# Kernel optimization log

Hardware: AMD Instinct MI355X
Metric: run time of the kernel (lower is better)

## Reference

```python
import jax, jax.numpy as jnp
import numpy as np

B, N, QD = 2, 2048, 1024
HEADS, DIM_HEAD = 16, 64
INNER = HEADS * DIM_HEAD  # 1024
SCALE = DIM_HEAD ** -0.5


def setup_inputs() -> dict:
    key = jax.random.key(0)
    ks = jax.random.split(key, 8)
    x = jax.random.normal(ks[0], (B, N, QD), dtype=jnp.float32)
    bias = jax.random.normal(ks[1], (B, N, N), dtype=jnp.float32)
    mask = jax.random.randint(ks[2], (B, N), 0, 2) > 0
    # parameters (nn.Linear stores weight [out, in]; we keep [in, out] and matmul x @ W)
    Wq = jax.random.normal(ks[3], (QD, INNER), dtype=jnp.float32) * (QD ** -0.5)
    Wkv = jax.random.normal(ks[4], (QD, 2 * INNER), dtype=jnp.float32) * (QD ** -0.5)
    Wo = jax.random.normal(ks[5], (INNER, QD), dtype=jnp.float32) * (INNER ** -0.5)
    bo = jax.random.normal(ks[6], (QD,), dtype=jnp.float32) * 0.01
    return {"x": x, "bias": bias, "mask": mask, "Wq": Wq, "Wkv": Wkv, "Wo": Wo, "bo": bo}


def reference(x, bias, mask, Wq, Wkv, Wo, bo):
    b, n, _ = x.shape
    q = x @ Wq                      # [b, n, inner]
    kv = x @ Wkv                    # [b, n, 2*inner] (context defaults to x)
    k, v = jnp.split(kv, 2, axis=-1)
    # split heads: [b, h, n, d]
    split = lambda t: t.reshape(b, n, HEADS, DIM_HEAD).transpose(0, 2, 1, 3)
    q, k, v = split(q), split(k), split(v)
    sim = jnp.einsum('bhid,bhjd->bhij', q, k) * SCALE   # [b, h, n, n]
    sim = sim + bias[:, None, :, :]                      # additive bias broadcast over heads
    max_neg = -jnp.finfo(sim.dtype).max
    sim = jnp.where(mask[:, None, None, :], sim, max_neg)  # per-key mask
    attn = jax.nn.softmax(sim, axis=-1)
    out = jnp.einsum('bhij,bhjd->bhid', attn, v)         # [b, h, n, d]
    out = out.transpose(0, 2, 1, 3).reshape(b, n, INNER)  # merge heads
    return out @ Wo + bo
```

## Files before the change

kernel.cpp:

```cpp
#include <hip/hip_runtime.h>
#include <hip/hip_bf16.h>
#include <stdint.h>

#define B_     2
#define N_     2048
#define QD_    1024
#define H_     16
#define DH_    64
#define INNER_ 1024
#define SCALE_ 0.125f

typedef unsigned short u16;
typedef __attribute__((ext_vector_type(8))) short bf16x8;
typedef __attribute__((ext_vector_type(4))) float f32x4;
typedef __attribute__((ext_vector_type(4))) unsigned short u16x4;
typedef __attribute__((ext_vector_type(8))) unsigned short u16x8;

#define GLD16(gp, lp) __builtin_amdgcn_global_load_lds( \
    (const __attribute__((address_space(1))) unsigned int*)(gp), \
    (__attribute__((address_space(3))) unsigned int*)(lp), 16, 0, 0)

__device__ inline u16 f2bf(float f) {
    union { float f; uint32_t u; } c; c.f = f;
    uint32_t r = c.u + 0x7FFFu + ((c.u >> 16) & 1u);
    return (u16)(r >> 16);
}
__device__ inline float bf2f(u16 s) {
    union { uint32_t u; float f; } c; c.u = ((uint32_t)s) << 16;
    return c.f;
}
__device__ inline void split2(float v, u16 &h, u16 &l) {
    u16 hs = f2bf(v);
    h = hs;
    l = f2bf(v - bf2f(hs));
}
__device__ inline unsigned pk2(float a, float b) {
    float2 f; f.x = a; f.y = b;
    union { __hip_bfloat162 v; unsigned u; } c;
    c.v = __float22bfloat162_rn(f);
    return c.u;
}
__device__ inline float f4get(const float4& v, int r) {
    return r == 0 ? v.x : r == 1 ? v.y : r == 2 ? v.z : v.w;
}

__global__ __launch_bounds__(256) void prep_kernel(
    const float* __restrict__ x, u16* __restrict__ xh, u16* __restrict__ xl,
    const float* __restrict__ Wq, const float* __restrict__ Wkv, const float* __restrict__ Wo,
    u16* __restrict__ wTh, u16* __restrict__ wTl,
    u16* __restrict__ woTh, u16* __restrict__ woTl)
{
    __shared__ float t[32][33];
    const int blk = blockIdx.x, tid = threadIdx.x;
    if (blk < 4096) {
        int idx = blk * 256 + tid;
        float4 v = ((const float4*)x)[idx];
        u16x4 hv, lv; u16 h, l;
        split2(v.x, h, l); hv.x = h; lv.x = l;
        split2(v.y, h, l); hv.y = h; lv.y = l;
        split2(v.z, h, l); hv.z = h; lv.z = l;
        split2(v.w, h, l); hv.w = h; lv.w = l;
        ((u16x4*)xh)[idx] = hv;
        ((u16x4*)xl)[idx] = lv;
        return;
    }
    int local = blk - 4096;
    const float* src; u16 *dhi, *dlo; int C, bx, by;
    if (local < 1024)      { src = Wq;  dhi = wTh;                dlo = wTl;                C = 1024; by = local >> 5; bx = local & 31; }
    else if (local < 3072) { int l2 = local - 1024; src = Wkv; dhi = wTh + 1024 * 1024; dlo = wTl + 1024 * 1024; C = 2048; by = l2 >> 6; bx = l2 & 63; }
    else                   { int l2 = local - 3072; src = Wo;  dhi = woTh;               dlo = woTl;               C = 1024; by = l2 >> 5; bx = l2 & 31; }
    const int x0 = bx * 32, y0 = by * 32;
    const int tx = tid & 31, ty = tid >> 5;
    for (int yy = ty; yy < 32; yy += 8)
        t[yy][tx] = src[(size_t)(y0 + yy) * C + x0 + tx];
    __syncthreads();
    for (int i = ty; i < 32; i += 8) {
        float v = t[tx][i];
        u16 h, l; split2(v, h, l);
        size_t o = (size_t)(x0 + i) * 1024 + y0 + tx;
        dhi[o] = h; dlo[o] = l;
    }
}

__device__ inline void bias_read(int T, int bkoff, int bl16,
                                 const float* __restrict__ bias,
                                 const int* __restrict__ mask,
                                 float4 bR[4], int4& bM)
{
    int bb2 = T >> 10, rest = T & 1023;
    int k0b = (rest & 31) * 64, q0 = (rest >> 5) * 64;
    int kk = k0b + bkoff;
    bM = *(const int4*)&mask[bb2 * N_ + kk];
#pragma unroll
    for (int m = 0; m < 4; m++)
        bR[m] = *(const float4*)&bias[((size_t)bb2 * N_ + q0 + m * 16 + bl16) * N_ + kk];
}
__device__ inline void bias_store(int T, int bwvr, int blane, int bhf,
                                  const float4 bR[4], const int4& bM,
                                  u16* __restrict__ bsw)
{
    int bb2 = T >> 10, rest = T & 1023;
    int k0b = (rest & 31) * 64, q0 = (rest >> 5) * 64;
    int wv = ((k0b >> 5) & 3) + bwvr;
    const u16 NEG = f2bf(-1e30f);
    const int mok[4] = { bM.x, bM.y, bM.z, bM.w };
    u16x8 o0, o1;
#pragma unroll
    for (int i = 0; i < 8; i++) {
        int m = i >> 2, r = i & 3;
        o0[i] = mok[r] ? f2bf(f4get(bR[m], r)) : NEG;
    }
#pragma unroll
    for (int i = 0; i < 8; i++) {
        int m = 2 + (i >> 2), r = i & 3;
        o1[i] = mok[r] ? f2bf(f4get(bR[m], r)) : NEG;
    }
    size_t ob = ((((size_t)bb2 * 32 + (q0 >> 6)) * 16 + (k0b >> 7)) * 4 + wv) * 2048
                + (size_t)blane * 32 + bhf * 16;
    *(u16x8*)&bsw[ob]     = o0;
    *(u16x8*)&bsw[ob + 8] = o1;
}

__global__ __launch_bounds__(256) void gemm_qkv_bias(
    int mode,
    const u16* __restrict__ Ah, const u16* __restrict__ Al,
    const u16* __restrict__ Bh,
    u16* __restrict__ qh,
    u16* __restrict__ kb, u16* __restrict__ vT,
    const float* __restrict__ bias, const int* __restrict__ mask,
    u16* __restrict__ bsw)
{
    __shared__ __align__(16) char smem[49152];
    const int tid = threadIdx.x;

    if (mode == 2) {
        const int bid = blockIdx.x;
        const int bp = tid >> 1, bhf = tid & 1;
        const int blane = bp & 63, bquad = blane >> 4, bl16 = blane & 15;
        const int bwvr = bp >> 6;
        const int bkoff = bwvr * 32 + bquad * 8 + bhf * 4;
        float4 bR[4]; int4 bM;
        bias_read(bid, bkoff, bl16, bias, mask, bR, bM);
        bias_store(bid, bwvr, blane, bhf, bR, bM, bsw);
        return;
    }
    const int gid = blockIdx.x;

    const int wave = tid >> 6, lane = tid & 63;
    const int quad = lane >> 4, l16 = lane & 15;
    const int wm = wave >> 1, wn = wave & 1;
    const int bx = gid % 24, by = gid / 24;
    const int bm = by * 128, bn = bx * 128;
    const bool comp = (bx < 8);

    f32x4 acc[4][4];
#pragma unroll
    for (int i = 0; i < 4; i++)
#pragma unroll
        for (int j = 0; j < 4; j++) acc[i][j] = (f32x4){0.f, 0.f, 0.f, 0.f};

    const int row0 = tid >> 2, g4 = tid & 3;
    const int r1 = row0, r2 = row0 + 64;
    const int gc1 = (g4 ^ (r1 & 3)) * 8, gc2 = (g4 ^ (r2 & 3)) * 8;
    const size_t a1 = (size_t)(bm + r1) * 1024 + gc1, a2 = (size_t)(bm + r2) * 1024 + gc2;
    const size_t b1 = (size_t)(bn + r1) * 1024 + gc1, b2 = (size_t)(bn + r2) * 1024 + gc2;
    const int ldsw = wave * 1024;

    auto issue = [&](char* base, int kn) {
        GLD16(Ah + a1 + kn, base + ldsw);
        GLD16(Ah + a2 + kn, base + 4096 + ldsw);
        GLD16(Bh + b1 + kn, base + 16384 + ldsw);
        GLD16(Bh + b2 + kn, base + 20480 + ldsw);
        if (comp) {
            GLD16(Al + a1 + kn, base + 8192 + ldsw);
            GLD16(Al + a2 + kn, base + 12288 + ldsw);
        }
    };

    const int bp = tid >> 1, bhf = tid & 1;
    const int blane = bp & 63, bquad = blane >> 4, bl16 = blane & 15;
    const int bwvr = bp >> 6;
    const int bkoff = bwvr * 32 + bquad * 8 + bhf * 4;
    float4 bR[4]; int4 bM;

    issue(smem, 0);
    int cur = 0;
    for (int k0 = 0; k0 < 1024; k0 += 32) {
        __syncthreads();
        char* cb_ = smem + cur * 24576;
        if (k0 + 32 < 1024) issue(smem + (cur ^ 1) * 24576, k0 + 32);
        if (mode == 1) {
            const int kstep = k0 >> 5;
            if (kstep == 3)  bias_read (gid,        bkoff, bl16, bias, mask, bR, bM);
            if (kstep == 7)  bias_store(gid,        bwvr, blane, bhf, bR, bM, bsw);
            if (kstep == 11) bias_read (gid + 768,  bkoff, bl16, bias, mask, bR, bM);
            if (kstep == 15) bias_store(gid + 768,  bwvr, blane, bhf, bR, bM, bsw);
            if (kstep == 19 && gid < 512) bias_read (gid + 1536, bkoff, bl16, bias, mask, bR, bM);
            if (kstep == 23 && gid < 512) bias_store(gid + 1536, bwvr, blane, bhf, bR, bM, bsw);
        }
        const u16* cAh = (const u16*)cb_;
        const u16* cAl = (const u16*)(cb_ + 8192);
        const u16* cBh = (const u16*)(cb_ + 16384);
        bf16x8 fah[4], fal[4], fbh[4];
#pragma unroll
        for (int s = 0; s < 4; s++) {
            int ra = wm * 64 + s * 16 + l16;
            int rb = wn * 64 + s * 16 + l16;
            int ca = (quad ^ (ra & 3)) * 8;
            int cb = (quad ^ (rb & 3)) * 8;
            fah[s] = *(const bf16x8*)&cAh[ra * 32 + ca];
            fbh[s] = *(const bf16x8*)&cBh[rb * 32 + cb];
            if (comp) fal[s] = *(const bf16x8*)&cAl[ra * 32 + ca];
        }
#pragma unroll
        for (int sm = 0; sm < 4; sm++)
#pragma unroll
            for (int sn = 0; sn < 4; sn++) {
                acc[sm][sn] = __builtin_amdgcn_mfma_f32_16x16x32_bf16(fah[sm], fbh[sn], acc[sm][sn], 0, 0, 0);
                if (comp)
                    acc[sm][sn] = __builtin_amdgcn_mfma_f32_16x16x32_bf16(fal[sm], fbh[sn], acc[sm][sn], 0, 0, 0);
            }
        cur ^= 1;
    }
#pragma unroll
    for (int sm = 0; sm < 4; sm++) {
        int rowb = bm + wm * 64 + sm * 16 + quad * 4;
        int bb = rowb >> 11, i0 = rowb & 2047;
#pragma unroll
        for (int sn = 0; sn < 4; sn++) {
            int col = bn + wn * 64 + sn * 16 + l16;
            int region = col >> 10;
            int hh = (col >> 6) & 15;
            int d = col & 63;
            if (region == 0) {
#pragma unroll
                for (int r = 0; r < 4; r++) {
                    size_t o = (((size_t)(bb * H_ + hh)) * N_ + i0 + r) * DH_ + d;
                    qh[o] = f2bf(acc[sm][sn][r] * SCALE_);
                }
            } else if (region == 1) {
#pragma unroll
                for (int r = 0; r < 4; r++) {
                    size_t o = (((size_t)(bb * H_ + hh)) * N_ + i0 + r) * DH_ + d;
                    kb[o] = f2bf(acc[sm][sn][r]);
                }
            } else {
                u16x4 pv;
#pragma unroll
                for (int r = 0; r < 4; r++) pv[r] = f2bf(acc[sm][sn][r]);
                *(u16x4*)&vT[(((size_t)(bb * H_ + hh)) * DH_ + d) * N_ + i0] = pv;
            }
        }
    }
}

__global__ __launch_bounds__(256) void gemm_out(
    const u16* __restrict__ Ab,
    const u16* __restrict__ Bh,
    const float* __restrict__ bo, float* __restrict__ out)
{
    __shared__ __align__(16) char smem[24576];
    const int tid = threadIdx.x;
    const int wave = tid >> 6, lane = tid & 63;
    const int quad = lane >> 4, l16 = lane & 15;
    const int wm = wave >> 1, wn = wave & 1;
    const int bm = blockIdx.y * 128, bn = blockIdx.x * 64;

    f32x4 acc[4][2];
#pragma unroll
    for (int i = 0; i < 4; i++)
#pragma unroll
        for (int j = 0; j < 2; j++) acc[i][j] = (f32x4){0.f, 0.f, 0.f, 0.f};

    const int row0 = tid >> 2, g4 = tid & 3;
    const int r1 = row0, r2 = row0 + 64;
    const int gc1 = (g4 ^ (r1 & 3)) * 8, gc2 = (g4 ^ (r2 & 3)) * 8;
    const size_t a1 = (size_t)(bm + r1) * 1024 + gc1, a2 = (size_t)(bm + r2) * 1024 + gc2;
    const size_t bgo = (size_t)(bn + r1) * 1024 + gc1;
    const int ldsw = wave * 1024;

    auto issue = [&](char* base, int kn) {
        GLD16(Ab + a1 + kn, base + ldsw);
        GLD16(Ab + a2 + kn, base + 4096 + ldsw);
        GLD16(Bh + bgo + kn, base + 8192 + ldsw);
    };

    issue(smem, 0);
    int cur = 0;
    for (int k0 = 0; k0 < 1024; k0 += 32) {
        __syncthreads();
        char* cb_ = smem + cur * 12288;
        if (k0 + 32 < 1024) issue(smem + (cur ^ 1) * 12288, k0 + 32);
        const u16* cA  = (const u16*)cb_;
        const u16* cBh = (const u16*)(cb_ + 8192);
        bf16x8 fa[4], fbh[2];
#pragma unroll
        for (int s = 0; s < 4; s++) {
            int ra = wm * 64 + s * 16 + l16;
            int ca = (quad ^ (ra & 3)) * 8;
            fa[s] = *(const bf16x8*)&cA[ra * 32 + ca];
        }
#pragma unroll
        for (int s = 0; s < 2; s++) {
            int rb = wn * 32 + s * 16 + l16;
            int cb = (quad ^ (rb & 3)) * 8;
            fbh[s] = *(const bf16x8*)&cBh[rb * 32 + cb];
        }
#pragma unroll
        for (int sm = 0; sm < 4; sm++)
#pragma unroll
            for (int sn = 0; sn < 2; sn++)
                acc[sm][sn] = __builtin_amdgcn_mfma_f32_16x16x32_bf16(fa[sm], fbh[sn], acc[sm][sn], 0, 0, 0);
        cur ^= 1;
    }
#pragma unroll
    for (int sm = 0; sm < 4; sm++) {
        int rowb = bm + wm * 64 + sm * 16 + quad * 4;
#pragma unroll
        for (int sn = 0; sn < 2; sn++) {
            int col = bn + wn * 32 + sn * 16 + l16;
            float bv = bo[col];
#pragma unroll
            for (int r = 0; r < 4; r++)
                out[(size_t)(rowb + r) * 1024 + col] = acc[sm][sn][r] + bv;
        }
    }
}

__global__ __launch_bounds__(256, 2) void attn_kernel(
    const u16* __restrict__ qh,
    const u16* __restrict__ kb, const u16* __restrict__ vT,
    const u16* __restrict__ bsw, u16* __restrict__ ob)
{
    __shared__ __align__(16) char smem[35328];
    float* rO = (float*)smem;
    float* rL = (float*)(smem + 34816);

    const int bh = blockIdx.y, b = bh >> 4, h = bh & 15;
    const int qt = blockIdx.x, qbase = qt * 64;
    const int tid = threadIdx.x, wave = tid >> 6, lane = tid & 63;
    const int quad = lane >> 4, l16 = lane & 15;

    bf16x8 aq[4][2];
#pragma unroll
    for (int m = 0; m < 4; m++) {
        size_t qo = ((size_t)bh * N_ + qbase + m * 16 + l16) * DH_ + quad * 8;
        aq[m][0] = *(const bf16x8*)&qh[qo];
        aq[m][1] = *(const bf16x8*)&qh[qo + 32];
    }
    f32x4 Oacc[4][4], lacc[4];
#pragma unroll
    for (int m = 0; m < 4; m++) {
        lacc[m] = (f32x4){0.f, 0.f, 0.f, 0.f};
#pragma unroll
        for (int nd = 0; nd < 4; nd++) Oacc[m][nd] = (f32x4){0.f, 0.f, 0.f, 0.f};
    }
    bf16x8 ones;
#pragma unroll
    for (int i = 0; i < 8; i++) ones[i] = (short)0x3F80;

    const int kperm = (l16 >> 2) * 8 + (l16 & 3);
    const size_t kbase0 = ((size_t)bh * N_ + wave * 32 + kperm) * DH_ + quad * 8;
    const size_t vbase0 = ((size_t)bh * DH_ + l16) * N_ + (wave * 4 + quad) * 8;
    const size_t bswb = (size_t)(b * 32 + qt) * 131072 + (size_t)wave * 2048
                        + (size_t)lane * 32;

    bf16x8 kc[2][2], vc[4];
    u16x8 cB[4];
#pragma unroll
    for (int n = 0; n < 2; n++)
#pragma unroll
        for (int s = 0; s < 2; s++)
            kc[n][s] = *(const bf16x8*)&kb[kbase0 + (size_t)(n * 4) * DH_ + s * 32];
#pragma unroll
    for (int nd = 0; nd < 4; nd++)
        vc[nd] = *(const bf16x8*)&vT[vbase0 + (size_t)(nd * 16) * N_];
#pragma unroll
    for (int c = 0; c < 4; c++) cB[c] = *(const u16x8*)&bsw[bswb + c * 8];

#pragma unroll
    for (int jt = 0; jt < 16; jt++) {
        bf16x8 kn_[2][2], vn_[4]; u16x8 nB[4];
        if (jt < 15) {
            int j0n = (jt + 1) * 128;
#pragma unroll
            for (int n = 0; n < 2; n++)
#pragma unroll
                for (int s = 0; s < 2; s++)
                    kn_[n][s] = *(const bf16x8*)&kb[kbase0 + (size_t)(j0n + n * 4) * DH_ + s * 32];
#pragma unroll
            for (int nd = 0; nd < 4; nd++)
                vn_[nd] = *(const bf16x8*)&vT[vbase0 + (size_t)(nd * 16) * N_ + j0n];
            size_t bb = bswb + (size_t)(jt + 1) * 8192;
#pragma unroll
            for (int c = 0; c < 4; c++) nB[c] = *(const u16x8*)&bsw[bb + c * 8];
        }
#pragma unroll
        for (int m = 0; m < 4; m++) {
            f32x4 S0 = (f32x4){0.f, 0.f, 0.f, 0.f};
            f32x4 S1 = (f32x4){0.f, 0.f, 0.f, 0.f};
#pragma unroll
            for (int s = 0; s < 2; s++) {
                S0 = __builtin_amdgcn_mfma_f32_16x16x32_bf16(kc[0][s], aq[m][s], S0, 0, 0, 0);
                S1 = __builtin_amdgcn_mfma_f32_16x16x32_bf16(kc[1][s], aq[m][s], S1, 0, 0, 0);
            }
            float p0[4], p1[4];
#pragma unroll
            for (int r = 0; r < 4; r++) {
                p0[r] = __expf(S0[r] + bf2f(cB[m >> 1][(m & 1) * 4 + r]));
                p1[r] = __expf(S1[r] + bf2f(cB[2 + (m >> 1)][(m & 1) * 4 + r]));
            }
            union { bf16x8 v; unsigned w[4]; } pa;
            pa.w[0] = pk2(p0[0], p0[1]);
            pa.w[1] = pk2(p0[2], p0[3]);
            pa.w[2] = pk2(p1[0], p1[1]);
            pa.w[3] = pk2(p1[2], p1[3]);
            lacc[m] = __builtin_amdgcn_mfma_f32_16x16x32_bf16(pa.v, ones, lacc[m], 0, 0, 0);
#pragma unroll
            for (int nd = 0; nd < 4; nd++)
                Oacc[m][nd] = __builtin_amdgcn_mfma_f32_16x16x32_bf16(pa.v, vc[nd], Oacc[m][nd], 0, 0, 0);
        }
        if (jt < 15) {
#pragma unroll
            for (int n = 0; n < 2; n++)
#pragma unroll
                for (int s = 0; s < 2; s++) kc[n][s] = kn_[n][s];
#pragma unroll
            for (int nd = 0; nd < 4; nd++) vc[nd] = vn_[nd];
#pragma unroll
            for (int c = 0; c < 4; c++) cB[c] = nB[c];
        }
    }

    if (wave >= 2) {
        int slot = wave - 2;
#pragma unroll
        for (int m = 0; m < 4; m++) {
#pragma unroll
            for (int nd = 0; nd < 4; nd++)
#pragma unroll
                for (int r = 0; r < 4; r++)
                    rO[(slot * 64 + m * 16 + quad * 4 + r) * 68 + nd * 16 + l16] = Oacc[m][nd][r];
            if (l16 == 0)
#pragma unroll
                for (int r = 0; r < 4; r++)
                    rL[slot * 64 + m * 16 + quad * 4 + r] = lacc[m][r];
        }
    }
    __syncthreads();
    if (wave < 2) {
        int slot = wave;
#pragma unroll
        for (int m = 0; m < 4; m++) {
#pragma unroll
            for (int nd = 0; nd < 4; nd++)
#pragma unroll
                for (int r = 0; r < 4; r++) {
                    int idx = (slot * 64 + m * 16 + quad * 4 + r) * 68 + nd * 16 + l16;
                    rO[idx] += Oacc[m][nd][r];
                }
            if (l16 == 0)
#pragma unroll
                for (int r = 0; r < 4; r++)
                    rL[slot * 64 + m * 16 + quad * 4 + r] += lacc[m][r];
        }
    }
    __syncthreads();
    {
        const int q = tid >> 2, dg = (tid & 3) * 16;
        float l = rL[q] + rL[64 + q];
        float inv = 1.f / l;
        f32x4 s[4];
#pragma unroll
        for (int i4 = 0; i4 < 4; i4++) {
            s[i4] = *(const f32x4*)&rO[(size_t)q * 68 + dg + i4 * 4];
            f32x4 v = *(const f32x4*)&rO[(size_t)(64 + q) * 68 + dg + i4 * 4];
            s[i4] += v;
        }
        size_t obase = ((size_t)b * N_ + qbase + q) * INNER_ + h * 64 + dg;
#pragma unroll
        for (int i4 = 0; i4 < 4; i4++) {
            u16x4 o4;
#pragma unroll
            for (int r = 0; r < 4; r++) o4[r] = f2bf(s[i4][r] * inv);
            *(u16x4*)&ob[obase + i4 * 4] = o4;
        }
    }
}

extern "C" void kernel_launch(void* const* d_in, const int* in_sizes, int n_in,
                              void* d_out, int out_size, void* d_ws, size_t ws_size,
                              hipStream_t stream)
{
    const float* x    = (const float*)d_in[0];
    const float* bias = (const float*)d_in[1];
    const int*   mask = (const int*)d_in[2];
    const float* Wq   = (const float*)d_in[3];
    const float* Wkv  = (const float*)d_in[4];
    const float* Wo   = (const float*)d_in[5];
    const float* bo   = (const float*)d_in[6];
    float* out = (float*)d_out;

    char* w = (char*)d_ws;
    const size_t MB = 1024 * 1024;
    u16* q_h   = (u16*)(w);
    u16* k_b   = (u16*)(w + 16 * MB);
    u16* v_T   = (u16*)(w + 24 * MB);
    u16* xs_h  = (u16*)(w + 32 * MB);
    u16* xs_l  = (u16*)(w + 40 * MB);
    u16* wT_h  = (u16*)(w + 48 * MB);
    u16* wT_l  = (u16*)(w + 54 * MB);
    u16* woT_h = (u16*)(w + 60 * MB);
    u16* woT_l = (u16*)(w + 62 * MB);
    u16* o_b   = (u16*)(w + 64 * MB);

    const size_t bsw_bytes = (size_t)2 * N_ * N_ * sizeof(u16);
    const bool concurrent = ws_size >= 72 * MB + bsw_bytes;

    prep_kernel<<<8192, 256, 0, stream>>>(x, xs_h, xs_l, Wq, Wkv, Wo, wT_h, wT_l, woT_h, woT_l);

    if (concurrent) {
        u16* bsw = (u16*)(w + 72 * MB);
        gemm_qkv_bias<<<768, 256, 0, stream>>>(1, xs_h, xs_l, wT_h,
                                               q_h, k_b, v_T, bias, mask, bsw);
        attn_kernel<<<dim3(32, 32), 256, 0, stream>>>(q_h, k_b, v_T, bsw, o_b);
    } else {
        u16* bsw = (u16*)(w + 32 * MB);
        gemm_qkv_bias<<<768, 256, 0, stream>>>(0, xs_h, xs_l, wT_h,
                                               q_h, k_b, v_T, bias, mask, bsw);
        gemm_qkv_bias<<<2048, 256, 0, stream>>>(2, xs_h, xs_l, wT_h,
                                                q_h, k_b, v_T, bias, mask, bsw);
        attn_kernel<<<dim3(32, 32), 256, 0, stream>>>(q_h, k_b, v_T, bsw, o_b);
    }
    gemm_out<<<dim3(16, 32), 256, 0, stream>>>(o_b, woT_h, bo, out);
}
```

Measured before the change: 287.0 us.

## Stage K/V tiles through swizzled LDS with coalesced loads and reschedule bias prefetch

The attention kernel now loads each 128-key K and V^T tile cooperatively with coalesced row-contiguous global loads into padded/XOR-swizzled shared memory, then reads MFMA fragments from LDS. Before, each wave fetched its fragments with scattered per-lane global loads. Register prefetch of the next tile overlaps with compute, at the cost of two barriers per iteration and a rolled outer loop. Separately, the bias read/store steps in the projection GEMM are spread further apart to hide global latency.

```diff
diff --git a/kernel.cpp b/kernel.cpp
--- a/kernel.cpp
+++ b/kernel.cpp
@@ -191,12 +191,12 @@
         if (k0 + 32 < 1024) issue(smem + (cur ^ 1) * 24576, k0 + 32);
         if (mode == 1) {
             const int kstep = k0 >> 5;
-            if (kstep == 3)  bias_read (gid,        bkoff, bl16, bias, mask, bR, bM);
-            if (kstep == 7)  bias_store(gid,        bwvr, blane, bhf, bR, bM, bsw);
+            if (kstep == 1)  bias_read (gid,        bkoff, bl16, bias, mask, bR, bM);
+            if (kstep == 9)  bias_store(gid,        bwvr, blane, bhf, bR, bM, bsw);
             if (kstep == 11) bias_read (gid + 768,  bkoff, bl16, bias, mask, bR, bM);
-            if (kstep == 15) bias_store(gid + 768,  bwvr, blane, bhf, bR, bM, bsw);
-            if (kstep == 19 && gid < 512) bias_read (gid + 1536, bkoff, bl16, bias, mask, bR, bM);
-            if (kstep == 23 && gid < 512) bias_store(gid + 1536, bwvr, blane, bhf, bR, bM, bsw);
+            if (kstep == 19) bias_store(gid + 768,  bwvr, blane, bhf, bR, bM, bsw);
+            if (kstep == 21 && gid < 512) bias_read (gid + 1536, bkoff, bl16, bias, mask, bR, bM);
+            if (kstep == 29 && gid < 512) bias_store(gid + 1536, bwvr, blane, bhf, bR, bM, bsw);
         }
         const u16* cAh = (const u16*)cb_;
         const u16* cAl = (const u16*)(cb_ + 8192);
@@ -327,12 +327,17 @@
     }
 }
 
+#define LDK 72
+#define LDV 128
+
 __global__ __launch_bounds__(256, 2) void attn_kernel(
     const u16* __restrict__ qh,
     const u16* __restrict__ kb, const u16* __restrict__ vT,
     const u16* __restrict__ bsw, u16* __restrict__ ob)
 {
     __shared__ __align__(16) char smem[35328];
+    u16* sK  = (u16*)smem;
+    u16* sVt = (u16*)(smem + 18432);
     float* rO = (float*)smem;
     float* rL = (float*)(smem + 34816);
 
@@ -359,50 +364,65 @@
 #pragma unroll
     for (int i = 0; i < 8; i++) ones[i] = (short)0x3F80;
 
-    const int kperm = (l16 >> 2) * 8 + (l16 & 3);
-    const size_t kbase0 = ((size_t)bh * N_ + wave * 32 + kperm) * DH_ + quad * 8;
-    const size_t vbase0 = ((size_t)bh * DH_ + l16) * N_ + (wave * 4 + quad) * 8;
+    const int rK = tid >> 3, cK = (tid & 7) * 8;
+    const int sigK = ((rK & 4) << 2) + ((rK >> 3) << 2) + (rK & 3);
+    const int rV = tid >> 4;
+    const int vg = tid & 15;
+    const int cV = vg * 8;
+    const int vsw = (vg ^ (rV & 7)) * 8;
+    const int vrg = ((wave * 4 + quad) ^ (l16 & 7)) * 8;
+    const size_t kgbase = (size_t)bh * N_ * DH_;
+    const size_t vgbase = (size_t)bh * DH_ * N_;
     const size_t bswb = (size_t)(b * 32 + qt) * 131072 + (size_t)wave * 2048
                         + (size_t)lane * 32;
 
-    bf16x8 kc[2][2], vc[4];
-    u16x8 cB[4];
-#pragma unroll
-    for (int n = 0; n < 2; n++)
-#pragma unroll
-        for (int s = 0; s < 2; s++)
-            kc[n][s] = *(const bf16x8*)&kb[kbase0 + (size_t)(n * 4) * DH_ + s * 32];
-#pragma unroll
-    for (int nd = 0; nd < 4; nd++)
-        vc[nd] = *(const bf16x8*)&vT[vbase0 + (size_t)(nd * 16) * N_];
+    bf16x8 pK[4], pV[4];
+    u16x8 cB[4], nB[4];
+#pragma unroll
+    for (int it = 0; it < 4; it++) {
+        pK[it] = *(const bf16x8*)&kb[kgbase + (size_t)(rK + it * 32) * DH_ + cK];
+        pV[it] = *(const bf16x8*)&vT[vgbase + (size_t)(rV + it * 16) * N_ + cV];
+    }
 #pragma unroll
     for (int c = 0; c < 4; c++) cB[c] = *(const u16x8*)&bsw[bswb + c * 8];
 
-#pragma unroll
     for (int jt = 0; jt < 16; jt++) {
-        bf16x8 kn_[2][2], vn_[4]; u16x8 nB[4];
-        if (jt < 15) {
-            int j0n = (jt + 1) * 128;
-#pragma unroll
-            for (int n = 0; n < 2; n++)
-#pragma unroll
-                for (int s = 0; s < 2; s++)
-                    kn_[n][s] = *(const bf16x8*)&kb[kbase0 + (size_t)(j0n + n * 4) * DH_ + s * 32];
-#pragma unroll
-            for (int nd = 0; nd < 4; nd++)
-                vn_[nd] = *(const bf16x8*)&vT[vbase0 + (size_t)(nd * 16) * N_ + j0n];
-            size_t bb = bswb + (size_t)(jt + 1) * 8192;
+#pragma unroll
+        for (int it = 0; it < 4; it++) {
+            *(bf16x8*)&sK[(it * 32 + sigK) * LDK + cK] = pK[it];
+            *(bf16x8*)&sVt[(rV + it * 16) * LDV + vsw] = pV[it];
+        }
+        __syncthreads();
+        {
+            int jn = (jt + 1) & 15;
+            int j0n = jn * 128;
+#pragma unroll
+            for (int it = 0; it < 4; it++) {
+                pK[it] = *(const bf16x8*)&kb[kgbase + (size_t)(j0n + rK + it * 32) * DH_ + cK];
+                pV[it] = *(const bf16x8*)&vT[vgbase + (size_t)(rV + it * 16) * N_ + j0n + cV];
+            }
+            size_t bb = bswb + (size_t)jn * 8192;
 #pragma unroll
             for (int c = 0; c < 4; c++) nB[c] = *(const u16x8*)&bsw[bb + c * 8];
         }
+        bf16x8 kf[2][2], vf[4];
+#pragma unroll
+        for (int n = 0; n < 2; n++)
+#pragma unroll
+            for (int s = 0; s < 2; s++)
+                kf[n][s] = *(const bf16x8*)&sK[(wave * 32 + n * 16 + l16) * LDK + s * 32 + quad * 8];
+#pragma unroll
+        for (int nd = 0; nd < 4; nd++)
+            vf[nd] = *(const bf16x8*)&sVt[(nd * 16 + l16) * LDV + vrg];
+
 #pragma unroll
         for (int m = 0; m < 4; m++) {
             f32x4 S0 = (f32x4){0.f, 0.f, 0.f, 0.f};
             f32x4 S1 = (f32x4){0.f, 0.f, 0.f, 0.f};
 #pragma unroll
             for (int s = 0; s < 2; s++) {
-                S0 = __builtin_amdgcn_mfma_f32_16x16x32_bf16(kc[0][s], aq[m][s], S0, 0, 0, 0);
-                S1 = __builtin_amdgcn_mfma_f32_16x16x32_bf16(kc[1][s], aq[m][s], S1, 0, 0, 0);
+                S0 = __builtin_amdgcn_mfma_f32_16x16x32_bf16(kf[0][s], aq[m][s], S0, 0, 0, 0);
+                S1 = __builtin_amdgcn_mfma_f32_16x16x32_bf16(kf[1][s], aq[m][s], S1, 0, 0, 0);
             }
             float p0[4], p1[4];
 #pragma unroll
@@ -418,18 +438,11 @@
             lacc[m] = __builtin_amdgcn_mfma_f32_16x16x32_bf16(pa.v, ones, lacc[m], 0, 0, 0);
 #pragma unroll
             for (int nd = 0; nd < 4; nd++)
-                Oacc[m][nd] = __builtin_amdgcn_mfma_f32_16x16x32_bf16(pa.v, vc[nd], Oacc[m][nd], 0, 0, 0);
-        }
-        if (jt < 15) {
-#pragma unroll
-            for (int n = 0; n < 2; n++)
-#pragma unroll
-                for (int s = 0; s < 2; s++) kc[n][s] = kn_[n][s];
-#pragma unroll
-            for (int nd = 0; nd < 4; nd++) vc[nd] = vn_[nd];
-#pragma unroll
-            for (int c = 0; c < 4; c++) cB[c] = nB[c];
-        }
+                Oacc[m][nd] = __builtin_amdgcn_mfma_f32_16x16x32_bf16(pa.v, vf[nd], Oacc[m][nd], 0, 0, 0);
+        }
+#pragma unroll
+        for (int c = 0; c < 4; c++) cB[c] = nB[c];
+        __syncthreads();
     }
 
     if (wave >= 2) {
```

After: 266.3 us. 1.08x faster.
